# Kernel tuning notes

Measured on AMD Instinct MI355X. Metric: run time of the kernel, lower is better.

The kernel has to match this reference:

```python
import jax, jax.numpy as jnp
import numpy as np

L, H, N, F, E, FF, OUT, B = 4, 8, 1024, 128, 128, 512, 64, 32


def setup_inputs() -> dict:
    key = jax.random.key(0)
    ks = jax.random.split(key, 16)
    s = 0.02
    return {
        "x": jax.random.normal(ks[0], (B, N, F), jnp.float32),
        "adj": jax.random.randint(ks[1], (N, N), 0, 2, jnp.int32),
        "Ws": jax.random.normal(ks[2], (L, H, E, F), jnp.float32) * s,
        "bs": jnp.zeros((L, H, E), jnp.float32),
        "As": jax.random.normal(ks[3], (L, H, 2 * E, N), jnp.float32) * s,
        "W1": jax.random.normal(ks[4], (L, FF, F), jnp.float32) * s,
        "b1": jnp.zeros((L, FF), jnp.float32),
        "W2": jax.random.normal(ks[5], (L, F, FF), jnp.float32) * s,
        "b2": jnp.zeros((L, F), jnp.float32),
        "g1": jnp.ones((L, F), jnp.float32),
        "be1": jnp.zeros((L, F), jnp.float32),
        "g2": jnp.ones((L, F), jnp.float32),
        "be2": jnp.zeros((L, F), jnp.float32),
        "Wo": jax.random.normal(ks[6], (OUT, N * F), jnp.float32) * s,
        "bo": jnp.zeros((OUT,), jnp.float32),
    }


def _ln(x, g, b, eps=1e-5):
    m = jnp.mean(x, axis=-1, keepdims=True)
    v = jnp.mean((x - m) ** 2, axis=-1, keepdims=True)
    return (x - m) / jnp.sqrt(v + eps) * g + b


def reference(x, adj, Ws, bs, As, W1, b1, W2, b2, g1, be1, g2, be2, Wo, bo):
    # mask[j, i] = 1 if j is a neighbor of i (adj_matrix[:, i] > 0 in torch source)
    mask = (adj > 0).astype(x.dtype)
    E_ = Ws.shape[2]
    for l in range(Ws.shape[0]):
        # per-head projection: h [B, H, N, E]
        h = jnp.einsum('bnf,hef->bhne', x, Ws[l]) + bs[l][None, :, None, :]
        # score[b,h,i] = h_i . a[:E, i] + (sum_{j in N(i)} h_j) . a[E:, i]
        s1 = jnp.einsum('bhne,hen->bhn', h, As[l][:, :E_, :])
        hn = jnp.einsum('jn,bhje->bhne', mask, h)  # neighbor sums
        s2 = jnp.einsum('bhne,hen->bhn', hn, As[l][:, E_:, :])
        score = s1 + s2  # [B, H, N]
        # attention row i is the constant score[b,h,i] broadcast over columns,
        # so attention @ h == score[...,None] * h.sum(over nodes)
        hsum = h.sum(axis=2)  # [B, H, E]
        hp = score[..., None] * hsum[:, :, None, :]  # [B, H, N, E]
        att = jax.nn.leaky_relu(hp, 0.01).sum(axis=1)  # sum over heads -> [B, N, F]
        x = _ln(x + att, g1[l], be1[l])
        ff = jax.nn.relu(x @ W1[l].T + b1[l]) @ W2[l].T + b2[l]
        x = _ln(x + ff, g2[l], be2[l])
    flat = x.reshape(x.shape[0], -1)  # [B, N*F]
    return jax.nn.relu(flat) @ Wo.T + bo
```

## Files before the change

### kernel.cpp

```cpp
#include <hip/hip_runtime.h>

#define L_ 4
#define H_ 8
#define Nn 1024
#define F_ 128
#define E_ 128
#define FF_ 512
#define OUT_ 64
#define B_ 32
#define KTOT (Nn * F_)

typedef unsigned short u16;
typedef __bf16 bf16_t;
typedef __attribute__((ext_vector_type(8))) __bf16 bf16x8;
typedef __attribute__((ext_vector_type(4))) float f32x4;

__device__ __forceinline__ u16 f2b(float v) {
    bf16_t h = (bf16_t)v;
    return __builtin_bit_cast(u16, h);
}
__device__ __forceinline__ float b2f(u16 u) {
    unsigned v = (unsigned)u << 16;
    return __builtin_bit_cast(float, v);
}

typedef const __attribute__((address_space(1))) void* gvp;
typedef __attribute__((address_space(3))) void* lvp;
__device__ __forceinline__ void gll16(const void* g, void* l) {
    __builtin_amdgcn_global_load_lds((gvp)g, (lvp)l, 16, 0, 0);
}

template <int R>
__device__ __forceinline__ void stage(const u16* __restrict__ g, int ldg,
                                      u16* lds, int w, int l) {
    const int r8 = l >> 3, jq = l & 7;
#pragma unroll
    for (int i = 0; i < R / 32; ++i) {
        const int row0 = w * (R / 4) + i * 8;
        const int row = row0 + r8;
        gll16(g + (long)row * ldg + ((jq ^ (row & 7)) << 3), lds + row0 * 64);
    }
}

template <int BM, int BN, bool DUAL, int EPI, int BSH, bool GSWAP, bool DBUF>
__global__ __launch_bounds__(256) void k_mfma(
    const u16* __restrict__ A, int lda, long sAz,
    const u16* __restrict__ Bhp, const u16* __restrict__ Blp, int ldb, long sBz,
    const float* __restrict__ bias,
    float* __restrict__ Cf, u16* __restrict__ Cb, int ldc, long sCz, int K)
{
    constexpr int WN = (BN == 64) ? 1 : ((BM == 64) ? 4 : 2);
    constexpr int WM = 4 / WN;
    constexpr int SM = BM / WM, SN = BN / WN;
    constexpr int MF = SM / 16, NF = SN / 16;
    constexpr int BUFE = BM * 64 + (DUAL ? 2 : 1) * BN * 64;
    __shared__ __align__(16) u16 lds[BUFE * (DBUF ? 2 : 1)];
    const int t = threadIdx.x;
    const int w = t >> 6, l = t & 63, lr = l & 15, lg = l >> 4;
    const int wm0 = (w / WN) * SM, wn0 = (w % WN) * SN;
    const int bidm = GSWAP ? blockIdx.z : blockIdx.x;
    const int bidz = GSWAP ? blockIdx.x : blockIdx.z;
    const int m0 = bidm * BM, n0 = blockIdx.y * BN;
    A += BSH ? ((long)(bidz >> 1) * sAz + (long)(bidz & 1) * 128)
             : (long)bidz * sAz;
    Bhp += (long)(bidz >> BSH) * sBz;
    if (DUAL) Blp += (long)bidz * sBz;

    f32x4 acc[MF][NF] = {};

    auto stageAll = [&](u16* base, int k0) {
        stage<BM>(A + (long)m0 * lda + k0, lda, base, w, l);
        stage<BN>(Bhp + (long)n0 * ldb + k0, ldb, base + BM * 64, w, l);
        if (DUAL) stage<BN>(Blp + (long)n0 * ldb + k0, ldb, base + BM * 64 + BN * 64, w, l);
    };
    auto compute = [&](const u16* base) {
        const u16* Al = base;
        const u16* Bh = base + BM * 64;
        const u16* Bl = Bh + BN * 64;
#pragma unroll
        for (int ks = 0; ks < 2; ++ks) {
            bf16x8 af[MF], bh[NF], bl[NF];
            const int kq = ks * 4 + lg;
#pragma unroll
            for (int mf = 0; mf < MF; ++mf) {
                int row = wm0 + mf * 16 + lr;
                af[mf] = *reinterpret_cast<const bf16x8*>(&Al[row * 64 + ((kq ^ (row & 7)) << 3)]);
            }
#pragma unroll
            for (int nf = 0; nf < NF; ++nf) {
                int row = wn0 + nf * 16 + lr;
                int off = row * 64 + ((kq ^ (row & 7)) << 3);
                bh[nf] = *reinterpret_cast<const bf16x8*>(&Bh[off]);
                if (DUAL) bl[nf] = *reinterpret_cast<const bf16x8*>(&Bl[off]);
            }
#pragma unroll
            for (int mf = 0; mf < MF; ++mf)
#pragma unroll
                for (int nf = 0; nf < NF; ++nf) {
                    acc[mf][nf] = __builtin_amdgcn_mfma_f32_16x16x32_bf16(af[mf], bh[nf], acc[mf][nf], 0, 0, 0);
                    if (DUAL)
                        acc[mf][nf] = __builtin_amdgcn_mfma_f32_16x16x32_bf16(af[mf], bl[nf], acc[mf][nf], 0, 0, 0);
                }
        }
    };

    if (DBUF) {
        stageAll(lds, 0);
        __syncthreads();
        int cur = 0;
        for (int k0 = 0; k0 < K; k0 += 64) {
            if (k0 + 64 < K) stageAll(lds + (cur ^ 1) * BUFE, k0 + 64);
            compute(lds + cur * BUFE);
            __syncthreads();
            cur ^= 1;
        }
    } else {
        for (int k0 = 0; k0 < K; k0 += 64) {
            __syncthreads();
            stageAll(lds, k0);
            __syncthreads();
            compute(lds);
        }
    }

    float bv[NF];
    if (EPI == 1) {
#pragma unroll
        for (int nf = 0; nf < NF; ++nf) bv[nf] = bias[n0 + wn0 + nf * 16 + lr];
    }
    if (EPI == 1 || EPI == 3) Cb += (long)bidz * sCz;
    else                      Cf += (long)bidz * sCz;
#pragma unroll
    for (int mf = 0; mf < MF; ++mf)
#pragma unroll
        for (int nf = 0; nf < NF; ++nf)
#pragma unroll
            for (int r = 0; r < 4; ++r) {
                long row = m0 + wm0 + mf * 16 + lg * 4 + r;
                int col = n0 + wn0 + nf * 16 + lr;
                float v = acc[mf][nf][r];
                if (EPI == 1) Cb[row * ldc + col] = f2b(fmaxf(v + bv[nf], 0.f));
                else if (EPI == 3) Cb[row * ldc + col] = f2b(v);
                else Cf[row * ldc + col] = v;
            }
}

template <bool LAST>
__global__ __launch_bounds__(256) void k_ff_ln2(
    const u16* __restrict__ xb,
    const u16* __restrict__ W1b,
    const float* __restrict__ b1,
    const u16* __restrict__ W2b,
    const float* __restrict__ b2,
    float* __restrict__ xc,
    const float* __restrict__ g, const float* __restrict__ be,
    u16* __restrict__ xh,
    float* __restrict__ xsp,
    u16* __restrict__ xrb)
{
    __shared__ __align__(16) u16 lds[32768];
    const int t = threadIdx.x;
    const int w = t >> 6, l = t & 63, lr = l & 15, lg = l >> 4;
    const int wn0 = w * 32;
    const int m0 = blockIdx.x * 64;
    u16* A0 = lds;
    u16* P0 = lds + 8192;
    u16* W0 = lds + 16384;

    stage<64>(xb + (long)m0 * F_,      F_, A0, w, l);
    stage<64>(xb + (long)m0 * F_ + 64, F_, A0 + 4096, w, l);

    f32x4 acc2[4][2] = {};
    for (int c = 0; c < 4; ++c) {
        __syncthreads();
        stage<128>(W1b + (long)(c * 128) * F_,      F_, W0, w, l);
        stage<128>(W1b + (long)(c * 128) * F_ + 64, F_, W0 + 8192, w, l);
        __syncthreads();
        f32x4 acc1[4][2] = {};
#pragma unroll
        for (int kh = 0; kh < 2; ++kh) {
            const u16* Ah = A0 + kh * 4096;
            const u16* Wh = W0 + kh * 8192;
#pragma unroll
            for (int ks = 0; ks < 2; ++ks) {
                const int kq = ks * 4 + lg;
                bf16x8 af[4], bfr[2];
#pragma unroll
                for (int mf = 0; mf < 4; ++mf) {
                    int row = mf * 16 + lr;
                    af[mf] = *reinterpret_cast<const bf16x8*>(&Ah[row * 64 + ((kq ^ (row & 7)) << 3)]);
                }
#pragma unroll
                for (int nf = 0; nf < 2; ++nf) {
                    int row = wn0 + nf * 16 + lr;
                    bfr[nf] = *reinterpret_cast<const bf16x8*>(&Wh[row * 64 + ((kq ^ (row & 7)) << 3)]);
                }
#pragma unroll
                for (int mf = 0; mf < 4; ++mf)
#pragma unroll
                    for (int nf = 0; nf < 2; ++nf)
                        acc1[mf][nf] = __builtin_amdgcn_mfma_f32_16x16x32_bf16(af[mf], bfr[nf], acc1[mf][nf], 0, 0, 0);
            }
        }
        float b1v[2] = { b1[c * 128 + wn0 + lr], b1[c * 128 + wn0 + 16 + lr] };
#pragma unroll
        for (int mf = 0; mf < 4; ++mf)
#pragma unroll
            for (int nf = 0; nf < 2; ++nf)
#pragma unroll
                for (int r = 0; r < 4; ++r) {
                    int row = mf * 16 + lg * 4 + r;
                    int sp = (row ^ (row >> 3)) & 7;
                    int cc = wn0 + nf * 16 + lr;
                    int c6 = cc & 63;
                    float v = fmaxf(acc1[mf][nf][r] + b1v[nf], 0.f);
                    P0[(cc >> 6) * 4096 + row * 64 + (((c6 >> 3) ^ sp) << 3) + (c6 & 7)] = f2b(v);
                }
        __syncthreads();
        stage<128>(W2b + c * 128,      FF_, W0, w, l);
        stage<128>(W2b + c * 128 + 64, FF_, W0 + 8192, w, l);
        __syncthreads();
#pragma unroll
        for (int kh = 0; kh < 2; ++kh) {
            const u16* Ph = P0 + kh * 4096;
            const u16* Wh = W0 + kh * 8192;
#pragma unroll
            for (int ks = 0; ks < 2; ++ks) {
                const int kq = ks * 4 + lg;
                bf16x8 af[4], bfr[2];
#pragma unroll
                for (int mf = 0; mf < 4; ++mf) {
                    int row = mf * 16 + lr;
                    int sp = (row ^ (row >> 3)) & 7;
                    af[mf] = *reinterpret_cast<const bf16x8*>(&Ph[row * 64 + ((kq ^ sp) << 3)]);
                }
#pragma unroll
                for (int nf = 0; nf < 2; ++nf) {
                    int row = wn0 + nf * 16 + lr;
                    bfr[nf] = *reinterpret_cast<const bf16x8*>(&Wh[row * 64 + ((kq ^ (row & 7)) << 3)]);
                }
#pragma unroll
                for (int mf = 0; mf < 4; ++mf)
#pragma unroll
                    for (int nf = 0; nf < 2; ++nf)
                        acc2[mf][nf] = __builtin_amdgcn_mfma_f32_16x16x32_bf16(af[mf], bfr[nf], acc2[mf][nf], 0, 0, 0);
            }
        }
    }
    __syncthreads();
    float (*buf)[132] = (float(*)[132])lds;
    float (*ps)[128]  = (float(*)[128])((char*)lds + 34816);
    float bv[2] = { b2[wn0 + lr], b2[wn0 + 16 + lr] };
#pragma unroll
    for (int mf = 0; mf < 4; ++mf)
#pragma unroll
        for (int nf = 0; nf < 2; ++nf)
#pragma unroll
            for (int r = 0; r < 4; ++r)
                buf[mf * 16 + lg * 4 + r][wn0 + nf * 16 + lr] = acc2[mf][nf][r] + bv[nf];
    __syncthreads();
    const float gl0 = g[l], gl1 = g[l + 64], bl0 = be[l], bl1 = be[l + 64];
    float s0 = 0.f, s1 = 0.f;
#pragma unroll
    for (int rr = 0; rr < 16; ++rr) {
        const int row = w * 16 + rr;
        const long xb_ = (long)(m0 + row) * F_;
        float v0 = buf[row][l] + xc[xb_ + l];
        float v1 = buf[row][l + 64] + xc[xb_ + l + 64];
        float sum = v0 + v1;
#pragma unroll
        for (int o = 32; o; o >>= 1) sum += __shfl_xor(sum, o);
        const float mean = sum * (1.f / 128.f);
        const float d0 = v0 - mean, d1 = v1 - mean;
        float vs = d0 * d0 + d1 * d1;
#pragma unroll
        for (int o = 32; o; o >>= 1) vs += __shfl_xor(vs, o);
        const float rstd = rsqrtf(vs * (1.f / 128.f) + 1e-5f);
        float o0 = d0 * rstd * gl0 + bl0;
        float o1 = d1 * rstd * gl1 + bl1;
        if (LAST) {
            xrb[xb_ + l] = f2b(fmaxf(o0, 0.f));
            xrb[xb_ + l + 64] = f2b(fmaxf(o1, 0.f));
        } else {
            xc[xb_ + l] = o0;       xc[xb_ + l + 64] = o1;
            buf[row][l] = o0;       buf[row][l + 64] = o1;
            s0 += o0;               s1 += o1;
        }
    }
    if (!LAST) {
        ps[w][l] = s0; ps[w][l + 64] = s1;
        __syncthreads();
        const int b = m0 >> 10, nb0 = m0 & 1023, seg = (m0 >> 6) & 15;
        const int n8 = (t & 7) * 8, fb = t >> 3;
#pragma unroll
        for (int i = 0; i < 4; ++i) {
            const int f = fb + 32 * i;
            union { u16 u[8]; float4 v; } Hv;
#pragma unroll
            for (int j = 0; j < 8; ++j) Hv.u[j] = f2b(buf[n8 + j][f]);
            *reinterpret_cast<float4*>(&xh[((long)b * F_ + f) * Nn + nb0 + n8]) = Hv.v;
        }
        if (t < 128)
            xsp[((long)b * 16 + seg) * 128 + t] =
                ps[0][t] + ps[1][t] + ps[2][t] + ps[3][t];
    }
}

__global__ __launch_bounds__(256) void k_final_mfma(
    const u16* __restrict__ xrb, const u16* __restrict__ Wob,
    float* __restrict__ part)
{
    __shared__ __align__(16) u16 Al[32 * 512];
    const int c = blockIdx.x;
    const long k0 = (long)c * 512;
    const int t = threadIdx.x, w = t >> 6, l = t & 63, lr = l & 15, lg = l >> 4;
#pragma unroll
    for (int i = 0; i < 8; ++i) {
        int ch = i * 256 + t, row = ch >> 6, jq = ch & 63;
        *reinterpret_cast<float4*>(&Al[row * 512 + ((jq ^ (row & 7)) << 3)]) =
            *reinterpret_cast<const float4*>(&xrb[(long)row * KTOT + k0 + (jq << 3)]);
    }
    __syncthreads();
    f32x4 acc[2] = {};
    const u16* Bp = Wob + (long)(w * 16 + lr) * KTOT + k0 + lg * 8;
#pragma unroll
    for (int ks = 0; ks < 16; ++ks) {
        bf16x8 bfr = *reinterpret_cast<const bf16x8*>(Bp + ks * 32);
        const int j8 = ks * 4 + lg;
#pragma unroll
        for (int mf = 0; mf < 2; ++mf) {
            int row = mf * 16 + lr;
            bf16x8 af = *reinterpret_cast<const bf16x8*>(&Al[row * 512 + ((j8 ^ (row & 7)) << 3)]);
            acc[mf] = __builtin_amdgcn_mfma_f32_16x16x32_bf16(af, bfr, acc[mf], 0, 0, 0);
        }
    }
#pragma unroll
    for (int mf = 0; mf < 2; ++mf)
#pragma unroll
        for (int r = 0; r < 4; ++r) {
            int b = mf * 16 + lg * 4 + r, o = w * 16 + lr;
            part[((long)c * B_ + b) * OUT_ + o] = acc[mf][r];
        }
}

__global__ void k_final_reduce(const float* __restrict__ part,
                               const float* __restrict__ bo, float* __restrict__ out)
{
    int i = blockIdx.x * 256 + threadIdx.x;
    int o = i & 63;
    float s = bo[o];
    for (int c = 0; c < 256; ++c) s += part[(long)c * (B_ * OUT_) + i];
    out[i] = s;
}

__global__ __launch_bounds__(256) void k_maskT(const int* __restrict__ adj,
                                               u16* __restrict__ maskTb,
                                               int* __restrict__ degi)
{
    __shared__ u16 tl[64][65];
    const int j0 = blockIdx.x * 64, n0 = blockIdx.y * 64, t = threadIdx.x;
#pragma unroll
    for (int i = 0; i < 16; ++i) {
        int s = i * 256 + t, jl = s >> 6, nl = s & 63;
        tl[jl][nl] = (adj[(long)(j0 + jl) * Nn + n0 + nl] > 0) ? 0x3F80 : 0;
    }
    __syncthreads();
    if (t < 64) {
        int c = 0;
#pragma unroll
        for (int jl = 0; jl < 64; ++jl) c += (tl[jl][t] != 0);
        atomicAdd(&degi[n0 + t], c);
    }
#pragma unroll
    for (int i = 0; i < 16; ++i) {
        int s = i * 256 + t, nl = s >> 6, jl = s & 63;
        maskTb[(long)(n0 + nl) * Nn + j0 + jl] = tl[jl][nl];
    }
}

__global__ __launch_bounds__(256) void k_tpb(const float* __restrict__ in,
                                             u16* __restrict__ out, int R, int C)
{
    __shared__ float tl[64][65];
    const int c0 = blockIdx.x * 64, r0 = blockIdx.y * 64, t = threadIdx.x;
    in  += (long)blockIdx.z * R * C;
    out += (long)blockIdx.z * R * C;
#pragma unroll
    for (int i = 0; i < 16; ++i) {
        int s = i * 256 + t, rl = s >> 6, cl = s & 63;
        tl[rl][cl] = in[(long)(r0 + rl) * C + c0 + cl];
    }
    __syncthreads();
#pragma unroll
    for (int i = 0; i < 16; ++i) {
        int s = i * 256 + t, cl = s >> 6, rl = s & 63;
        out[(long)(c0 + cl) * R + r0 + rl] = f2b(tl[rl][cl]);
    }
}

__global__ void k_cvtW(const float* __restrict__ W1, const float* __restrict__ W2,
                       u16* __restrict__ W1b, u16* __restrict__ W2b)
{
    int i = blockIdx.x * 256 + threadIdx.x;
    W1b[i] = f2b(W1[i]);
    W2b[i] = f2b(W2[i]);
}

__global__ void k_cvtWo(const float* __restrict__ Wo, u16* __restrict__ Wob)
{
    long i = ((long)blockIdx.x * 256 + threadIdx.x) * 8;
    float4 a = *reinterpret_cast<const float4*>(&Wo[i]);
    float4 b = *reinterpret_cast<const float4*>(&Wo[i + 4]);
    union { u16 u[8]; float4 v; } r;
    r.u[0] = f2b(a.x); r.u[1] = f2b(a.y); r.u[2] = f2b(a.z); r.u[3] = f2b(a.w);
    r.u[4] = f2b(b.x); r.u[5] = f2b(b.y); r.u[6] = f2b(b.z); r.u[7] = f2b(b.w);
    *reinterpret_cast<float4*>(&Wob[i]) = r.v;
}

__global__ __launch_bounds__(256) void k_xpose(const float* __restrict__ x,
                                               u16* __restrict__ xh)
{
    __shared__ float tile[64][132];
    const int b = blockIdx.y, n0 = blockIdx.x * 64, t = threadIdx.x;
#pragma unroll
    for (int i = 0; i < 8; ++i) {
        int s = i * 256 + t, nl = s >> 5, f4 = (s & 31) << 2;
        float4 v = *reinterpret_cast<const float4*>(&x[((long)b * Nn + n0 + nl) * F_ + f4]);
        tile[nl][f4] = v.x; tile[nl][f4 + 1] = v.y;
        tile[nl][f4 + 2] = v.z; tile[nl][f4 + 3] = v.w;
    }
    __syncthreads();
    const int f = t >> 1, nb = (t & 1) << 5;
    const long ob = ((long)b * F_ + f) * Nn + n0 + nb;
    union { u16 u[8]; float4 v; } Hv;
#pragma unroll
    for (int i = 0; i < 32; i += 8) {
#pragma unroll
        for (int j = 0; j < 8; ++j) Hv.u[j] = f2b(tile[nb + i + j][f]);
        *reinterpret_cast<float4*>(&xh[ob + i]) = Hv.v;
    }
}

__global__ __launch_bounds__(256) void k_xs2(const float* __restrict__ x, float* __restrict__ xsp)
{
    __shared__ float sh[2][128];
    const int seg = blockIdx.x, b = blockIdx.y, t = threadIdx.x;
    const int f = t & 127, h2 = t >> 7;
    const float* p = x + ((long)b * Nn + seg * 64 + h2 * 32) * F_ + f;
    float s = 0.f;
    for (int i = 0; i < 32; ++i) s += p[(long)i * F_];
    sh[h2][f] = s;
    __syncthreads();
    if (t < 128) xsp[((long)b * 16 + seg) * 128 + t] = sh[0][t] + sh[1][t];
}

__global__ void k_hsum(const float* __restrict__ xsp, const float* __restrict__ Wl,
                       const float* __restrict__ bsl, float* __restrict__ hsum)
{
    __shared__ float xs[128];
    const int i = blockIdx.x * 256 + threadIdx.x;
    const int b = i >> 10;
    if (threadIdx.x < 128) {
        const float* xp = xsp + (long)b * 16 * 128 + threadIdx.x;
        float v = 0.f;
#pragma unroll
        for (int sg = 0; sg < 16; ++sg) v += xp[sg * 128];
        xs[threadIdx.x] = v;
    }
    __syncthreads();
    const int e = i & 127, h = (i >> 7) & 7;
    const float* w = Wl + ((long)h * E_ + e) * F_;
    float s = 0.f;
    for (int f = 0; f < F_; ++f) s += xs[f] * w[f];
    hsum[i] = s + (float)Nn * bsl[h * E_ + e];
}

__global__ void k_d12(const float* __restrict__ As, const float* __restrict__ bs,
                      float* __restrict__ d12all)
{
    const int lyr = blockIdx.y;
    const float* Asl = As + (long)lyr * H_ * 2 * E_ * Nn;
    const float* bsl = bs + (long)lyr * H_ * E_;
    int i = blockIdx.x * 256 + threadIdx.x;
    int n = i & 1023, h = (i >> 10) & 7, w = i >> 13;
    const float* a = Asl + ((long)h * 2 * E_ + (long)w * E_) * Nn + n;
    const float* bb = bsl + h * E_;
    float s = 0.f;
    for (int e = 0; e < E_; ++e) s += bb[e] * a[(long)e * Nn];
    d12all[(long)lyr * 2 * H_ * Nn + ((long)w * H_ + h) * Nn + n] = s;
}

__global__ __launch_bounds__(256) void k_score_ln1(
    float* __restrict__ x, const u16* __restrict__ y,
    const float* __restrict__ Ct, const float* __restrict__ d12,
    const int* __restrict__ degi, const float* __restrict__ hsum,
    const float* __restrict__ g, const float* __restrict__ be,
    u16* __restrict__ xb)
{
    const int n = blockIdx.x, t = threadIdx.x;
    __shared__ float c1[H_][128], c2[H_][128];
    __shared__ float sbs[H_];
#pragma unroll
    for (int i = 0; i < 4; ++i) {
        int s = i * 256 + t, h = s >> 7, f = s & 127;
        c1[h][f] = Ct[((long)(2 * h) * Nn + n) * F_ + f];
        c2[h][f] = Ct[((long)(2 * h + 1) * Nn + n) * F_ + f];
    }
    if (t < H_) sbs[t] = d12[(long)t * Nn + n] + (float)degi[n] * d12[(long)(H_ + t) * Nn + n];
    __syncthreads();
    const int w = t >> 6, l = t & 63;
    const float gl0 = g[l], gl1 = g[l + 64], bl0 = be[l], bl1 = be[l + 64];
    for (int bi = 0; bi < 8; ++bi) {
        const int b = w * 8 + bi;
        const long base = ((long)b * Nn + n) * F_;
        float x0 = x[base + l], x1 = x[base + l + 64];
        float y0 = b2f(y[base + l]), y1 = b2f(y[base + l + 64]);
        float a0 = 0.f, a1 = 0.f;
#pragma unroll
        for (int h = 0; h < H_; ++h) {
            float p = x0 * c1[h][l] + x1 * c1[h][l + 64]
                    + y0 * c2[h][l] + y1 * c2[h][l + 64];
#pragma unroll
            for (int o = 32; o; o >>= 1) p += __shfl_xor(p, o);
            float s = p + sbs[h];
            float h0 = hsum[((long)b * H_ + h) * E_ + l];
            float h1 = hsum[((long)b * H_ + h) * E_ + l + 64];
            float p0 = s * h0, p1 = s * h1;
            a0 += (p0 > 0.f ? p0 : 0.01f * p0);
            a1 += (p1 > 0.f ? p1 : 0.01f * p1);
        }
        float v0 = x0 + a0, v1 = x1 + a1;
        float sum = v0 + v1;
#pragma unroll
        for (int o = 32; o; o >>= 1) sum += __shfl_xor(sum, o);
        const float mean = sum * (1.f / 128.f);
        const float d0 = v0 - mean, d1 = v1 - mean;
        float vs = d0 * d0 + d1 * d1;
#pragma unroll
        for (int o = 32; o; o >>= 1) vs += __shfl_xor(vs, o);
        const float rstd = rsqrtf(vs * (1.f / 128.f) + 1e-5f);
        float o0 = d0 * rstd * gl0 + bl0;
        float o1 = d1 * rstd * gl1 + bl1;
        x[base + l] = o0;        x[base + l + 64] = o1;
        xb[base + l] = f2b(o0);  xb[base + l + 64] = f2b(o1);
    }
}

extern "C" void kernel_launch(void* const* d_in, const int* in_sizes, int n_in,
                              void* d_out, int out_size, void* d_ws, size_t ws_size,
                              hipStream_t stream)
{
    const float* x_in = (const float*)d_in[0];
    const int*   adj  = (const int*)d_in[1];
    const float* Ws   = (const float*)d_in[2];
    const float* bs   = (const float*)d_in[3];
    const float* As   = (const float*)d_in[4];
    const float* W1   = (const float*)d_in[5];
    const float* b1   = (const float*)d_in[6];
    const float* W2   = (const float*)d_in[7];
    const float* b2   = (const float*)d_in[8];
    const float* g1   = (const float*)d_in[9];
    const float* be1  = (const float*)d_in[10];
    const float* g2   = (const float*)d_in[11];
    const float* be2  = (const float*)d_in[12];
    const float* Wo   = (const float*)d_in[13];
    const float* bo   = (const float*)d_in[14];
    float* out = (float*)d_out;

    char* wsb = (char*)d_ws;
    u16*   maskTb = (u16*)wsb;
    float* xc     = (float*)(wsb + (2L << 20));
    u16*   yb     = (u16*)(wsb + (18L << 20));
    float* CtAll  = (float*)(wsb + (66L << 20));
    u16*   xb     = (u16*)(wsb + (98L << 20));
    u16*   xrb    = (u16*)(wsb + (106L << 20));
    u16*   Wob    = (u16*)(wsb + (114L << 20));
    float* part   = (float*)(wsb + (130L << 20));
    u16*   xTh    = (u16*)(wsb + (132L << 20));
    u16*   AsTb   = (u16*)(wsb + (148L << 20));
    u16*   WsTb   = (u16*)(wsb + (164L << 20));
    char*  S      = wsb + (166L << 20);
    int*   degi   = (int*)S;
    float* xsp    = (float*)(S + (4L << 10));
    float* hsum   = (float*)(S + (260L << 10));
    float* d12all = (float*)(S + (388L << 10));
    u16*   W1b    = (u16*)(S + (644L << 10));
    u16*   W2b    = (u16*)(S + (1156L << 10));

    hipMemsetAsync(degi, 0, Nn * sizeof(int), stream);
    hipMemcpyAsync(xc, x_in, sizeof(float) * (long)B_ * Nn * F_,
                   hipMemcpyDeviceToDevice, stream);
    k_maskT<<<dim3(16, 16), 256, 0, stream>>>(adj, maskTb, degi);
    k_cvtW<<<(L_ * FF_ * F_) / 256, 256, 0, stream>>>(W1, W2, W1b, W2b);
    k_cvtWo<<<(OUT_ * KTOT) / (256 * 8), 256, 0, stream>>>(Wo, Wob);
    k_tpb<<<dim3(16, 4, L_ * H_), 256, 0, stream>>>(As, AsTb, 2 * E_, Nn);
    k_tpb<<<dim3(2, 2, L_ * H_), 256, 0, stream>>>(Ws, WsTb, E_, F_);
    k_xpose<<<dim3(16, B_), 256, 0, stream>>>(x_in, xTh);
    k_xs2<<<dim3(16, B_), 256, 0, stream>>>(x_in, xsp);
    k_d12<<<dim3((2 * H_ * Nn) / 256, L_), 256, 0, stream>>>(As, bs, d12all);
    k_mfma<64, 128, false, 0, 1, false, false><<<dim3(16, 1, 64), 256, 0, stream>>>(
        AsTb, 2 * E_, (long)Nn * 2 * E_, WsTb, nullptr, E_, (long)F_ * E_,
        nullptr, CtAll, nullptr, F_, (long)Nn * F_, E_);

    for (int l = 0; l < L_; ++l) {
        const float* Wl  = Ws + (long)l * H_ * E_ * F_;
        const float* bsl = bs + (long)l * H_ * E_;

        k_mfma<128, 64, false, 3, 0, true, true><<<dim3(32, 2, 8), 256, 0, stream>>>(
            maskTb, Nn, 0L, xTh, nullptr, Nn, (long)F_ * Nn,
            nullptr, nullptr, yb, F_, (long)Nn * F_, Nn);

        k_hsum<<<(B_ * H_ * E_) / 256, 256, 0, stream>>>(xsp, Wl, bsl, hsum);
        k_score_ln1<<<Nn, 256, 0, stream>>>(
            xc, yb, CtAll + (long)l * 16 * Nn * F_, d12all + (long)l * 2 * H_ * Nn,
            degi, hsum, g1 + l * F_, be1 + l * F_, xb);
        if (l < L_ - 1)
            k_ff_ln2<false><<<512, 256, 0, stream>>>(
                xb, W1b + (long)l * FF_ * F_, b1 + l * FF_,
                W2b + (long)l * F_ * FF_, b2 + l * F_, xc,
                g2 + l * F_, be2 + l * F_, xTh, xsp, nullptr);
        else
            k_ff_ln2<true><<<512, 256, 0, stream>>>(
                xb, W1b + (long)l * FF_ * F_, b1 + l * FF_,
                W2b + (long)l * F_ * FF_, b2 + l * F_, xc,
                g2 + l * F_, be2 + l * F_, nullptr, nullptr, xrb);
    }

    k_final_mfma<<<256, 256, 0, stream>>>(xrb, Wob, part);
    k_final_reduce<<<(B_ * OUT_) / 256, 256, 0, stream>>>(part, bo, out);
}
```

Before: 368.5 us.

## Enlarge FFN+LN2 block to 128 rows with double-buffered W1/W2 staging

```diff
diff --git a/kernel.cpp b/kernel.cpp
--- a/kernel.cpp
+++ b/kernel.cpp
@@ -37,6 +37,17 @@
 #pragma unroll
     for (int i = 0; i < R / 32; ++i) {
         const int row0 = w * (R / 4) + i * 8;
+        const int row = row0 + r8;
+        gll16(g + (long)row * ldg + ((jq ^ (row & 7)) << 3), lds + row0 * 64);
+    }
+}
+
+__device__ __forceinline__ void stage128x64(const u16* __restrict__ g, int ldg,
+                                            u16* lds, int w, int l) {
+    const int r8 = l >> 3, jq = l & 7;
+#pragma unroll
+    for (int i = 0; i < 2; ++i) {
+        const int row0 = i * 64 + w * 8;
         const int row = row0 + r8;
         gll16(g + (long)row * ldg + ((jq ^ (row & 7)) << 3), lds + row0 * 64);
     }
@@ -146,7 +157,7 @@
 }
 
 template <bool LAST>
-__global__ __launch_bounds__(256) void k_ff_ln2(
+__global__ __launch_bounds__(512) void k_ff_ln2(
     const u16* __restrict__ xb,
     const u16* __restrict__ W1b,
     const float* __restrict__ b1,
@@ -158,49 +169,56 @@
     float* __restrict__ xsp,
     u16* __restrict__ xrb)
 {
-    __shared__ __align__(16) u16 lds[32768];
+    __shared__ __align__(16) u16 lds[65536];
     const int t = threadIdx.x;
     const int w = t >> 6, l = t & 63, lr = l & 15, lg = l >> 4;
-    const int wn0 = w * 32;
-    const int m0 = blockIdx.x * 64;
+    const int wr = w >> 2, wc = w & 3;
+    const int wn0 = wc * 32;
+    const int m0 = blockIdx.x * 128;
     u16* A0 = lds;
-    u16* P0 = lds + 8192;
-    u16* W0 = lds + 16384;
-
-    stage<64>(xb + (long)m0 * F_,      F_, A0, w, l);
-    stage<64>(xb + (long)m0 * F_ + 64, F_, A0 + 4096, w, l);
+    u16* P0 = lds + 16384;
+    u16* Wb0 = lds + 32768;
+    u16* Wb1 = lds + 49152;
+
+    stage128x64(xb + (long)m0 * F_,      F_, A0, w, l);
+    stage128x64(xb + (long)m0 * F_ + 64, F_, A0 + 8192, w, l);
+    stage128x64(W1b,      F_, Wb0, w, l);
+    stage128x64(W1b + 64, F_, Wb0 + 8192, w, l);
+    float xcr[32];
+#pragma unroll
+    for (int rr = 0; rr < 16; ++rr) {
+        const long xof = (long)(m0 + w * 16 + rr) * F_;
+        xcr[rr * 2]     = xc[xof + l];
+        xcr[rr * 2 + 1] = xc[xof + l + 64];
+    }
+    __syncthreads();
 
     f32x4 acc2[4][2] = {};
     for (int c = 0; c < 4; ++c) {
-        __syncthreads();
-        stage<128>(W1b + (long)(c * 128) * F_,      F_, W0, w, l);
-        stage<128>(W1b + (long)(c * 128) * F_ + 64, F_, W0 + 8192, w, l);
-        __syncthreads();
+        stage128x64(W2b + c * 128,      FF_, Wb1, w, l);
+        stage128x64(W2b + c * 128 + 64, FF_, Wb1 + 8192, w, l);
         f32x4 acc1[4][2] = {};
 #pragma unroll
-        for (int kh = 0; kh < 2; ++kh) {
-            const u16* Ah = A0 + kh * 4096;
-            const u16* Wh = W0 + kh * 8192;
-#pragma unroll
-            for (int ks = 0; ks < 2; ++ks) {
-                const int kq = ks * 4 + lg;
-                bf16x8 af[4], bfr[2];
-#pragma unroll
-                for (int mf = 0; mf < 4; ++mf) {
-                    int row = mf * 16 + lr;
-                    af[mf] = *reinterpret_cast<const bf16x8*>(&Ah[row * 64 + ((kq ^ (row & 7)) << 3)]);
-                }
-#pragma unroll
-                for (int nf = 0; nf < 2; ++nf) {
-                    int row = wn0 + nf * 16 + lr;
-                    bfr[nf] = *reinterpret_cast<const bf16x8*>(&Wh[row * 64 + ((kq ^ (row & 7)) << 3)]);
-                }
-#pragma unroll
-                for (int mf = 0; mf < 4; ++mf)
-#pragma unroll
-                    for (int nf = 0; nf < 2; ++nf)
-                        acc1[mf][nf] = __builtin_amdgcn_mfma_f32_16x16x32_bf16(af[mf], bfr[nf], acc1[mf][nf], 0, 0, 0);
+        for (int s = 0; s < 4; ++s) {
+            const int kh = s >> 1, kq = (s & 1) * 4 + lg;
+            bf16x8 af[4], bfr[2];
+#pragma unroll
+            for (int mf = 0; mf < 4; ++mf) {
+                int row = wr * 64 + mf * 16 + lr;
+                af[mf] = *reinterpret_cast<const bf16x8*>(
+                    &A0[kh * 8192 + row * 64 + ((kq ^ (row & 7)) << 3)]);
             }
+#pragma unroll
+            for (int nf = 0; nf < 2; ++nf) {
+                int row = wn0 + nf * 16 + lr;
+                bfr[nf] = *reinterpret_cast<const bf16x8*>(
+                    &Wb0[kh * 8192 + row * 64 + ((kq ^ (row & 7)) << 3)]);
+            }
+#pragma unroll
+            for (int mf = 0; mf < 4; ++mf)
+#pragma unroll
+                for (int nf = 0; nf < 2; ++nf)
+                    acc1[mf][nf] = __builtin_amdgcn_mfma_f32_16x16x32_bf16(af[mf], bfr[nf], acc1[mf][nf], 0, 0, 0);
         }
         float b1v[2] = { b1[c * 128 + wn0 + lr], b1[c * 128 + wn0 + 16 + lr] };
 #pragma unroll
@@ -209,47 +227,45 @@
             for (int nf = 0; nf < 2; ++nf)
 #pragma unroll
                 for (int r = 0; r < 4; ++r) {
-                    int row = mf * 16 + lg * 4 + r;
+                    int row = wr * 64 + mf * 16 + lg * 4 + r;
                     int sp = (row ^ (row >> 3)) & 7;
                     int cc = wn0 + nf * 16 + lr;
                     int c6 = cc & 63;
                     float v = fmaxf(acc1[mf][nf][r] + b1v[nf], 0.f);
-                    P0[(cc >> 6) * 4096 + row * 64 + (((c6 >> 3) ^ sp) << 3) + (c6 & 7)] = f2b(v);
+                    P0[(cc >> 6) * 8192 + row * 64 + (((c6 >> 3) ^ sp) << 3) + (c6 & 7)] = f2b(v);
                 }
         __syncthreads();
-        stage<128>(W2b + c * 128,      FF_, W0, w, l);
-        stage<128>(W2b + c * 128 + 64, FF_, W0 + 8192, w, l);
+        if (c < 3) {
+            stage128x64(W1b + (long)(c + 1) * 128 * F_,      F_, Wb0, w, l);
+            stage128x64(W1b + (long)(c + 1) * 128 * F_ + 64, F_, Wb0 + 8192, w, l);
+        }
+#pragma unroll
+        for (int s = 0; s < 4; ++s) {
+            const int kh = s >> 1, kq = (s & 1) * 4 + lg;
+            bf16x8 af[4], bfr[2];
+#pragma unroll
+            for (int mf = 0; mf < 4; ++mf) {
+                int row = wr * 64 + mf * 16 + lr;
+                int sp = (row ^ (row >> 3)) & 7;
+                af[mf] = *reinterpret_cast<const bf16x8*>(
+                    &P0[kh * 8192 + row * 64 + ((kq ^ sp) << 3)]);
+            }
+#pragma unroll
+            for (int nf = 0; nf < 2; ++nf) {
+                int row = wn0 + nf * 16 + lr;
+                bfr[nf] = *reinterpret_cast<const bf16x8*>(
+                    &Wb1[kh * 8192 + row * 64 + ((kq ^ (row & 7)) << 3)]);
+            }
+#pragma unroll
+            for (int mf = 0; mf < 4; ++mf)
+#pragma unroll
+                for (int nf = 0; nf < 2; ++nf)
+                    acc2[mf][nf] = __builtin_amdgcn_mfma_f32_16x16x32_bf16(af[mf], bfr[nf], acc2[mf][nf], 0, 0, 0);
+        }
         __syncthreads();
-#pragma unroll
-        for (int kh = 0; kh < 2; ++kh) {
-            const u16* Ph = P0 + kh * 4096;
-            const u16* Wh = W0 + kh * 8192;
-#pragma unroll
-            for (int ks = 0; ks < 2; ++ks) {
-                const int kq = ks * 4 + lg;
-                bf16x8 af[4], bfr[2];
-#pragma unroll
-                for (int mf = 0; mf < 4; ++mf) {
-                    int row = mf * 16 + lr;
-                    int sp = (row ^ (row >> 3)) & 7;
-                    af[mf] = *reinterpret_cast<const bf16x8*>(&Ph[row * 64 + ((kq ^ sp) << 3)]);
-                }
-#pragma unroll
-                for (int nf = 0; nf < 2; ++nf) {
-                    int row = wn0 + nf * 16 + lr;
-                    bfr[nf] = *reinterpret_cast<const bf16x8*>(&Wh[row * 64 + ((kq ^ (row & 7)) << 3)]);
-                }
-#pragma unroll
-                for (int mf = 0; mf < 4; ++mf)
-#pragma unroll
-                    for (int nf = 0; nf < 2; ++nf)
-                        acc2[mf][nf] = __builtin_amdgcn_mfma_f32_16x16x32_bf16(af[mf], bfr[nf], acc2[mf][nf], 0, 0, 0);
-            }
-        }
-    }
-    __syncthreads();
+    }
     float (*buf)[132] = (float(*)[132])lds;
-    float (*ps)[128]  = (float(*)[128])((char*)lds + 34816);
+    float (*ps)[128]  = (float(*)[128])((char*)lds + 69632);
     float bv[2] = { b2[wn0 + lr], b2[wn0 + 16 + lr] };
 #pragma unroll
     for (int mf = 0; mf < 4; ++mf)
@@ -257,7 +273,7 @@
         for (int nf = 0; nf < 2; ++nf)
 #pragma unroll
             for (int r = 0; r < 4; ++r)
-                buf[mf * 16 + lg * 4 + r][wn0 + nf * 16 + lr] = acc2[mf][nf][r] + bv[nf];
+                buf[wr * 64 + mf * 16 + lg * 4 + r][wn0 + nf * 16 + lr] = acc2[mf][nf][r] + bv[nf];
     __syncthreads();
     const float gl0 = g[l], gl1 = g[l + 64], bl0 = be[l], bl1 = be[l + 64];
     float s0 = 0.f, s1 = 0.f;
@@ -265,8 +281,8 @@
     for (int rr = 0; rr < 16; ++rr) {
         const int row = w * 16 + rr;
         const long xb_ = (long)(m0 + row) * F_;
-        float v0 = buf[row][l] + xc[xb_ + l];
-        float v1 = buf[row][l + 64] + xc[xb_ + l + 64];
+        float v0 = buf[row][l] + xcr[rr * 2];
+        float v1 = buf[row][l + 64] + xcr[rr * 2 + 1];
         float sum = v0 + v1;
 #pragma unroll
         for (int o = 32; o; o >>= 1) sum += __shfl_xor(sum, o);
@@ -290,8 +306,8 @@
     if (!LAST) {
         ps[w][l] = s0; ps[w][l + 64] = s1;
         __syncthreads();
-        const int b = m0 >> 10, nb0 = m0 & 1023, seg = (m0 >> 6) & 15;
-        const int n8 = (t & 7) * 8, fb = t >> 3;
+        const int b = m0 >> 10, nb0 = m0 & 1023, seg = (m0 >> 7) & 7;
+        const int n8 = (t & 15) * 8, fb = t >> 4;
 #pragma unroll
         for (int i = 0; i < 4; ++i) {
             const int f = fb + 32 * i;
@@ -300,9 +316,12 @@
             for (int j = 0; j < 8; ++j) Hv.u[j] = f2b(buf[n8 + j][f]);
             *reinterpret_cast<float4*>(&xh[((long)b * F_ + f) * Nn + nb0 + n8]) = Hv.v;
         }
-        if (t < 128)
-            xsp[((long)b * 16 + seg) * 128 + t] =
-                ps[0][t] + ps[1][t] + ps[2][t] + ps[3][t];
+        if (t < 128) {
+            float s = 0.f;
+#pragma unroll
+            for (int k = 0; k < 8; ++k) s += ps[k][t];
+            xsp[((long)b * 8 + seg) * 128 + t] = s;
+        }
     }
 }
 
@@ -446,12 +465,12 @@
     __shared__ float sh[2][128];
     const int seg = blockIdx.x, b = blockIdx.y, t = threadIdx.x;
     const int f = t & 127, h2 = t >> 7;
-    const float* p = x + ((long)b * Nn + seg * 64 + h2 * 32) * F_ + f;
+    const float* p = x + ((long)b * Nn + seg * 128 + h2 * 64) * F_ + f;
     float s = 0.f;
-    for (int i = 0; i < 32; ++i) s += p[(long)i * F_];
+    for (int i = 0; i < 64; ++i) s += p[(long)i * F_];
     sh[h2][f] = s;
     __syncthreads();
-    if (t < 128) xsp[((long)b * 16 + seg) * 128 + t] = sh[0][t] + sh[1][t];
+    if (t < 128) xsp[((long)b * 8 + seg) * 128 + t] = sh[0][t] + sh[1][t];
 }
 
 __global__ void k_hsum(const float* __restrict__ xsp, const float* __restrict__ Wl,
@@ -461,10 +480,10 @@
     const int i = blockIdx.x * 256 + threadIdx.x;
     const int b = i >> 10;
     if (threadIdx.x < 128) {
-        const float* xp = xsp + (long)b * 16 * 128 + threadIdx.x;
+        const float* xp = xsp + (long)b * 8 * 128 + threadIdx.x;
         float v = 0.f;
 #pragma unroll
-        for (int sg = 0; sg < 16; ++sg) v += xp[sg * 128];
+        for (int sg = 0; sg < 8; ++sg) v += xp[sg * 128];
         xs[threadIdx.x] = v;
     }
     __syncthreads();
@@ -582,10 +601,10 @@
     char*  S      = wsb + (166L << 20);
     int*   degi   = (int*)S;
     float* xsp    = (float*)(S + (4L << 10));
-    float* hsum   = (float*)(S + (260L << 10));
-    float* d12all = (float*)(S + (388L << 10));
-    u16*   W1b    = (u16*)(S + (644L << 10));
-    u16*   W2b    = (u16*)(S + (1156L << 10));
+    float* hsum   = (float*)(S + (132L << 10));
+    float* d12all = (float*)(S + (260L << 10));
+    u16*   W1b    = (u16*)(S + (516L << 10));
+    u16*   W2b    = (u16*)(S + (1028L << 10));
 
     hipMemsetAsync(degi, 0, Nn * sizeof(int), stream);
     hipMemcpyAsync(xc, x_in, sizeof(float) * (long)B_ * Nn * F_,
@@ -596,7 +615,7 @@
     k_tpb<<<dim3(16, 4, L_ * H_), 256, 0, stream>>>(As, AsTb, 2 * E_, Nn);
     k_tpb<<<dim3(2, 2, L_ * H_), 256, 0, stream>>>(Ws, WsTb, E_, F_);
     k_xpose<<<dim3(16, B_), 256, 0, stream>>>(x_in, xTh);
-    k_xs2<<<dim3(16, B_), 256, 0, stream>>>(x_in, xsp);
+    k_xs2<<<dim3(8, B_), 256, 0, stream>>>(x_in, xsp);
     k_d12<<<dim3((2 * H_ * Nn) / 256, L_), 256, 0, stream>>>(As, bs, d12all);
     k_mfma<64, 128, false, 0, 1, false, false><<<dim3(16, 1, 64), 256, 0, stream>>>(
         AsTb, 2 * E_, (long)Nn * 2 * E_, WsTb, nullptr, E_, (long)F_ * E_,
@@ -615,12 +634,12 @@
             xc, yb, CtAll + (long)l * 16 * Nn * F_, d12all + (long)l * 2 * H_ * Nn,
             degi, hsum, g1 + l * F_, be1 + l * F_, xb);
         if (l < L_ - 1)
-            k_ff_ln2<false><<<512, 256, 0, stream>>>(
+            k_ff_ln2<false><<<256, 512, 0, stream>>>(
                 xb, W1b + (long)l * FF_ * F_, b1 + l * FF_,
                 W2b + (long)l * F_ * FF_, b2 + l * F_, xc,
                 g2 + l * F_, be2 + l * F_, xTh, xsp, nullptr);
         else
-            k_ff_ln2<true><<<512, 256, 0, stream>>>(
+            k_ff_ln2<true><<<256, 512, 0, stream>>>(
                 xb, W1b + (long)l * FF_ * F_, b1 + l * FF_,
                 W2b + (long)l * F_ * FF_, b2 + l * F_, xc,
                 g2 + l * F_, be2 + l * F_, nullptr, nullptr, xrb);
```

After: 372.7 us. Within noise of the previous version (+1.1%).
